# Kernel optimization log

Hardware: AMD Instinct MI355X
Metric: run time of the kernel (lower is better)

Reference implementation:

```python
import jax, jax.numpy as jnp
import numpy as np

COUNTS = (16, 8, 8)  # num_scale_layers from __init__


def _conv1d(x, w, b):
    # x: [B, C, L], w: [Cout, Cin, K] (torch Conv1d layout), valid padding, stride 1
    y = jax.lax.conv_general_dilated(
        x, w, window_strides=(1,), padding='VALID',
        dimension_numbers=('NCH', 'OIH', 'NCH'))
    return y + b[None, :, None]


def _maxpool3s2(x):
    # MaxPool1d(kernel=3, stride=2), valid padding
    return jax.lax.reduce_window(x, -jnp.inf, jax.lax.max,
                                 (1, 1, 3), (1, 1, 2), 'VALID')


def setup_inputs() -> dict:
    key = jax.random.key(0)
    ks = jax.random.split(key, 5)
    B, C, N = 64, 512, 64
    scale = 0.03  # ~1/sqrt(C*K), keeps deep relu-conv chain numerically sane
    x = jax.random.normal(ks[0], (B, C, N), jnp.float32)
    w1 = jax.random.normal(ks[1], (C, C, 1), jnp.float32) * scale
    b1 = jax.random.normal(ks[2], (C,), jnp.float32) * scale
    n_k2 = sum(COUNTS) - len(COUNTS)  # 29 kernel-size-2 convs
    w2 = jax.random.normal(ks[3], (n_k2, C, C, 2), jnp.float32) * scale
    b2 = jax.random.normal(ks[4], (n_k2, C), jnp.float32) * scale
    return {"x": x, "w1": w1, "b1": b1, "w2": w2, "b2": b2}


def reference(x, w1, b1, w2, b2):
    B, C, N = x.shape
    x2d = jnp.zeros((B, C, N, N), x.dtype)
    mask = np.eye(N, dtype=bool)  # static: indices are compile-time constants
    k2 = 0
    stride, offset = 1, 0
    for level, count in enumerate(COUNTS):
        for order in range(count):
            if level == 0 and order == 0:
                x = jax.nn.relu(_conv1d(x, w1, b1))
            elif level > 0 and order == 0:
                x = jax.nn.relu(_maxpool3s2(x))
            else:
                x = jax.nn.relu(_conv1d(x, w2[k2], b2[k2]))
                k2 += 1
            i = np.arange(0, N - offset, stride)
            j = np.arange(offset, N, stride)
            # scatter conv output onto strided diagonal of the 2D map
            x2d = x2d.at[:, :, i, j].set(x)
            mask[i, j] = True
            offset += stride
        offset += stride
        stride *= 2
    return x2d, jnp.asarray(mask)
```

## Files before the change

### kernel.cpp

```cpp
#include <hip/hip_runtime.h>

typedef _Float16 f16;
typedef f16 f16x8 __attribute__((ext_vector_type(8)));
typedef f16 f16x4 __attribute__((ext_vector_type(4)));
typedef f16 f16x2 __attribute__((ext_vector_type(2)));
typedef float f32x4 __attribute__((ext_vector_type(4)));

#define B_ 64
#define C_ 512
#define X2D_ELEMS ((size_t)134217728)
#define CHAIN_PITCH 1104

__device__ __forceinline__ int col_of(int i, int j) {
    const int d = j - i;
    if (d < 0) return -1;
    if (d <= 15) return 64 * d - (d * (d - 1)) / 2 + i;
    if (d >= 17 && d <= 31 && (d & 1) && !(i & 1)) {
        const int v = (d - 17) >> 1;
        return 904 + 24 * v - (v * (v - 1)) / 2 + (i >> 1);
    }
    if (d >= 35 && !((d - 35) & 3) && !(i & 3)) {
        const int v = (d - 35) >> 2;
        return 1068 + 8 * v - (v * (v - 1)) / 2 + (i >> 2);
    }
    return -1;
}

template<int K, int TAPS>
__global__ __launch_bounds__(256, 2)
void conv_fused(const f16* __restrict__ xin, int in_pitch, int cb_in,
                const f16* __restrict__ Wl, const float* __restrict__ bias,
                f16* __restrict__ chain, int cb_out,
                int Lin, int Lout, int G)
{
    __shared__ f16 Bs[64 * 512];
    const int tid = threadIdx.x, lane = tid & 63, wv = tid >> 6;
    const int b0 = blockIdx.x * G, m0 = blockIdx.y * 64;
    const int rows = G * Lin;

    for (int r = wv; r < rows; r += 4) {
        const int g = r / Lin, l = r - g * Lin;
        const f16* src = xin + (((size_t)(b0 + g) * in_pitch + cb_in + l) << 9);
        const f16x8 v = *(const f16x8*)(src + (lane << 3));
        *(f16x8*)&Bs[(r << 9) + ((lane ^ (r & 7)) << 3)] = v;
    }

    int vg[4], vl[4], row0[4]; bool val[4];
    #pragma unroll
    for (int nf = 0; nf < 4; nf++) {
        const int v = nf * 16 + (lane & 15);
        vg[nf] = v / Lout; vl[nf] = v - vg[nf] * Lout;
        val[nf] = vg[nf] < G;
        row0[nf] = val[nf] ? vg[nf] * Lin + vl[nf] : 0;
    }
    const int kg = lane >> 4;
    const f16* wp = Wl + (size_t)(m0 + wv * 16 + (lane & 15)) * K + (kg << 3);

    __syncthreads();

    f32x4 acc[4] = {};
    #pragma unroll 4
    for (int k0 = 0; k0 < K; k0 += 32) {
        const f16x8 af = *(const f16x8*)(wp + k0);
        const int t = (TAPS == 2 && k0 >= 512) ? 1 : 0;
        const int cchunk = (((TAPS == 2) ? (k0 & 511) : k0) >> 3) + kg;
        #pragma unroll
        for (int nf = 0; nf < 4; nf++) {
            const int r = row0[nf] + t;
            const f16x8 bf = *(const f16x8*)&Bs[(r << 9) + ((cchunk ^ (r & 7)) << 3)];
            acc[nf] = __builtin_amdgcn_mfma_f32_16x16x32_f16(af, bf, acc[nf], 0, 0, 0);
        }
    }

    const int co0 = m0 + wv * 16 + ((lane >> 4) << 2);
    const float4 bb = *(const float4*)&bias[co0];
    #pragma unroll
    for (int nf = 0; nf < 4; nf++) {
        if (!val[nf]) continue;
        f16x4 h;
        #pragma unroll
        for (int j = 0; j < 4; j++)
            h[j] = (f16)fmaxf(acc[nf][j] + ((const float*)&bb)[j], 0.0f);
        *(f16x4*)&chain[(((size_t)(b0 + vg[nf]) * CHAIN_PITCH + cb_out + vl[nf]) << 9) + co0] = h;
    }
}

__global__ void maxpool2(f16* __restrict__ chain, int cb_in, int cb_out)
{
    const int l = blockIdx.x, b = blockIdx.y, tid = threadIdx.x;
    const f16* s = chain + (((size_t)b * CHAIN_PITCH + cb_in + 2 * l) << 9) + 2 * tid;
    f16x2 o;
    o[0] = (f16)fmaxf(fmaxf(fmaxf((float)s[0], (float)s[512]), (float)s[1024]), 0.0f);
    o[1] = (f16)fmaxf(fmaxf(fmaxf((float)s[1], (float)s[513]), (float)s[1025]), 0.0f);
    *(f16x2*)&chain[(((size_t)b * CHAIN_PITCH + cb_out + l) << 9) + 2 * tid] = o;
}

__global__ void mask_kernel(float* __restrict__ mout)
{
    const int t = blockIdx.x * 256 + threadIdx.x;
    const int i = t >> 6, j = t & 63;
    mout[t] = (col_of(i, j) >= 0) ? 1.0f : 0.0f;
}

__global__ void wprep(const float* __restrict__ w1, const float* __restrict__ w2,
                      f16* __restrict__ Wf)
{
    size_t idx = (size_t)blockIdx.x * 256 + threadIdx.x;
    if (idx < 262144) {
        Wf[idx] = (f16)w1[idx];
    } else {
        idx -= 262144;
        const int k2 = idx >> 18;
        const int rem = idx & 262143;
        const int co = rem >> 9, ci = rem & 511;
        const float2 v = *(const float2*)&w2[((((size_t)k2 << 9) + co) << 10) + (ci << 1)];
        f16* base = Wf + 262144 + ((size_t)k2 << 19) + ((size_t)co << 10);
        base[ci] = (f16)v.x;
        base[512 + ci] = (f16)v.y;
    }
}

__global__ __launch_bounds__(256)
void xtrans(const float* __restrict__ x, f16* __restrict__ xT)
{
    __shared__ f16 t[64][20];
    const int s = blockIdx.x, b = blockIdx.y, tid = threadIdx.x;
    const int ci = tid >> 4, l0 = (tid & 15) << 2;
    const float4 v = *(const float4*)&x[(((size_t)b * C_ + s * 16 + ci) << 6) + l0];
    t[l0 + 0][ci] = (f16)v.x; t[l0 + 1][ci] = (f16)v.y;
    t[l0 + 2][ci] = (f16)v.z; t[l0 + 3][ci] = (f16)v.w;
    __syncthreads();
    const int l = tid >> 2, q = tid & 3;
    const f16x4 o = *(const f16x4*)&t[l][q << 2];
    *(f16x4*)&xT[((((size_t)b << 6) + l) << 9) + (s << 4) + (q << 2)] = o;
}

__global__ __launch_bounds__(256)
void assemble3(const f16* __restrict__ chain, float* __restrict__ x2d)
{
    __shared__ f16 J[64 * 512];
    const int tid = threadIdx.x, lane = tid & 63, wv = tid >> 6;
    const int i = blockIdx.x, b = blockIdx.y;

    for (int j = wv; j < 64; j += 4) {
        const int col = col_of(i, j);
        f16x8 v = {0, 0, 0, 0, 0, 0, 0, 0};
        if (col >= 0)
            v = *(const f16x8*)(chain + (((size_t)b * CHAIN_PITCH + col) << 9) + (lane << 3));
        *(f16x8*)&J[(j << 9) + ((lane ^ (j & 7)) << 3)] = v;
    }
    __syncthreads();

    const int jq = tid & 15, c0 = tid >> 4;
    float* dst0 = x2d + (((size_t)b * C_) << 12) + (i << 6) + (jq << 2);
    for (int ct = 0; ct < 32; ct++) {
        const int c = c0 + (ct << 4);
        const int cj = c >> 3;
        float4 o;
        #pragma unroll
        for (int jj = 0; jj < 4; jj++) {
            const int j = (jq << 2) + jj;
            ((float*)&o)[jj] = (float)J[(j << 9) + ((cj ^ (j & 7)) << 3) + (c & 7)];
        }
        *(float4*)(dst0 + ((size_t)c << 12)) = o;
    }
}

extern "C" void kernel_launch(void* const* d_in, const int* in_sizes, int n_in,
                              void* d_out, int out_size, void* d_ws, size_t ws_size,
                              hipStream_t stream)
{
    const float* x  = (const float*)d_in[0];
    const float* w1 = (const float*)d_in[1];
    const float* b1 = (const float*)d_in[2];
    const float* w2 = (const float*)d_in[3];
    const float* b2 = (const float*)d_in[4];
    float* x2d   = (float*)d_out;
    float* maskp = x2d + X2D_ELEMS;

    f16* chain = (f16*)d_ws;
    f16* Wf = (f16*)x2d;
    f16* xT = Wf + 262144 + (size_t)29 * 524288;

    mask_kernel<<<16, 256, 0, stream>>>(maskp);
    wprep<<<(30 * 262144) / 256, 256, 0, stream>>>(w1, w2, Wf);
    xtrans<<<dim3(32, B_), 256, 0, stream>>>(x, xT);

    const int counts[3] = {16, 8, 8};
    int L = 64, k2 = 0, cb = 0, prev = 0;
    for (int level = 0; level < 3; level++) {
        for (int order = 0; order < counts[level]; order++) {
            if (level == 0 && order == 0) {
                conv_fused<512, 1><<<dim3(64, 8), 256, 0, stream>>>(
                    xT, 64, 0, Wf, b1, chain, cb, 64, 64, 1);
            } else if (level > 0 && order == 0) {
                const int Lp = (L - 3) / 2 + 1;
                maxpool2<<<dim3(Lp, B_), 256, 0, stream>>>(chain, prev, cb);
                L = Lp;
            } else {
                const int Lout = L - 1;
                int G = 1;
                while ((G * 2) * Lout <= 64 && (G * 2) * L <= 64) G *= 2;
                conv_fused<1024, 2><<<dim3(64 / G, 8), 256, 0, stream>>>(
                    chain, CHAIN_PITCH, prev,
                    Wf + 262144 + (size_t)k2 * 524288, b2 + (size_t)k2 * C_,
                    chain, cb, L, Lout, G);
                k2++; L = Lout;
            }
            prev = cb; cb += L;
        }
    }
    assemble3<<<dim3(64, B_), 256, 0, stream>>>(chain, x2d);
}
```

Measured before the change: 652.0 us.

## Fuse all stages into one persistent cooperative kernel with grid syncs

```diff
diff --git a/kernel.cpp b/kernel.cpp
--- a/kernel.cpp
+++ b/kernel.cpp
@@ -1,4 +1,7 @@
 #include <hip/hip_runtime.h>
+#include <hip/hip_cooperative_groups.h>
+
+namespace cg = cooperative_groups;
 
 typedef _Float16 f16;
 typedef f16 f16x8 __attribute__((ext_vector_type(8)));
@@ -26,25 +29,20 @@
     return -1;
 }
 
-template<int K, int TAPS>
-__global__ __launch_bounds__(256, 2)
-void conv_fused(const f16* __restrict__ xin, int in_pitch, int cb_in,
-                const f16* __restrict__ Wl, const float* __restrict__ bias,
-                f16* __restrict__ chain, int cb_out,
-                int Lin, int Lout, int G)
-{
-    __shared__ f16 Bs[64 * 512];
+__device__ __forceinline__
+void conv_unit(f16* S, const f16* __restrict__ xin, int in_pitch, int cb_in,
+               const f16* __restrict__ Wl, const float* __restrict__ bias,
+               f16* __restrict__ chain, int cb_out,
+               int Lin, int Lout, int G, int K, int b0, int m0)
+{
     const int tid = threadIdx.x, lane = tid & 63, wv = tid >> 6;
-    const int b0 = blockIdx.x * G, m0 = blockIdx.y * 64;
     const int rows = G * Lin;
-
     for (int r = wv; r < rows; r += 4) {
         const int g = r / Lin, l = r - g * Lin;
         const f16* src = xin + (((size_t)(b0 + g) * in_pitch + cb_in + l) << 9);
         const f16x8 v = *(const f16x8*)(src + (lane << 3));
-        *(f16x8*)&Bs[(r << 9) + ((lane ^ (r & 7)) << 3)] = v;
-    }
-
+        *(f16x8*)&S[(r << 9) + ((lane ^ (r & 7)) << 3)] = v;
+    }
     int vg[4], vl[4], row0[4]; bool val[4];
     #pragma unroll
     for (int nf = 0; nf < 4; nf++) {
@@ -55,23 +53,20 @@
     }
     const int kg = lane >> 4;
     const f16* wp = Wl + (size_t)(m0 + wv * 16 + (lane & 15)) * K + (kg << 3);
-
     __syncthreads();
-
     f32x4 acc[4] = {};
     #pragma unroll 4
     for (int k0 = 0; k0 < K; k0 += 32) {
         const f16x8 af = *(const f16x8*)(wp + k0);
-        const int t = (TAPS == 2 && k0 >= 512) ? 1 : 0;
-        const int cchunk = (((TAPS == 2) ? (k0 & 511) : k0) >> 3) + kg;
+        const int t = (k0 >= 512) ? 1 : 0;
+        const int cchunk = ((k0 & 511) >> 3) + kg;
         #pragma unroll
         for (int nf = 0; nf < 4; nf++) {
             const int r = row0[nf] + t;
-            const f16x8 bf = *(const f16x8*)&Bs[(r << 9) + ((cchunk ^ (r & 7)) << 3)];
+            const f16x8 bf = *(const f16x8*)&S[(r << 9) + ((cchunk ^ (r & 7)) << 3)];
             acc[nf] = __builtin_amdgcn_mfma_f32_16x16x32_f16(af, bf, acc[nf], 0, 0, 0);
         }
     }
-
     const int co0 = m0 + wv * 16 + ((lane >> 4) << 2);
     const float4 bb = *(const float4*)&bias[co0];
     #pragma unroll
@@ -85,72 +80,19 @@
     }
 }
 
-__global__ void maxpool2(f16* __restrict__ chain, int cb_in, int cb_out)
-{
-    const int l = blockIdx.x, b = blockIdx.y, tid = threadIdx.x;
-    const f16* s = chain + (((size_t)b * CHAIN_PITCH + cb_in + 2 * l) << 9) + 2 * tid;
-    f16x2 o;
-    o[0] = (f16)fmaxf(fmaxf(fmaxf((float)s[0], (float)s[512]), (float)s[1024]), 0.0f);
-    o[1] = (f16)fmaxf(fmaxf(fmaxf((float)s[1], (float)s[513]), (float)s[1025]), 0.0f);
-    *(f16x2*)&chain[(((size_t)b * CHAIN_PITCH + cb_out + l) << 9) + 2 * tid] = o;
-}
-
-__global__ void mask_kernel(float* __restrict__ mout)
-{
-    const int t = blockIdx.x * 256 + threadIdx.x;
-    const int i = t >> 6, j = t & 63;
-    mout[t] = (col_of(i, j) >= 0) ? 1.0f : 0.0f;
-}
-
-__global__ void wprep(const float* __restrict__ w1, const float* __restrict__ w2,
-                      f16* __restrict__ Wf)
-{
-    size_t idx = (size_t)blockIdx.x * 256 + threadIdx.x;
-    if (idx < 262144) {
-        Wf[idx] = (f16)w1[idx];
-    } else {
-        idx -= 262144;
-        const int k2 = idx >> 18;
-        const int rem = idx & 262143;
-        const int co = rem >> 9, ci = rem & 511;
-        const float2 v = *(const float2*)&w2[((((size_t)k2 << 9) + co) << 10) + (ci << 1)];
-        f16* base = Wf + 262144 + ((size_t)k2 << 19) + ((size_t)co << 10);
-        base[ci] = (f16)v.x;
-        base[512 + ci] = (f16)v.y;
-    }
-}
-
-__global__ __launch_bounds__(256)
-void xtrans(const float* __restrict__ x, f16* __restrict__ xT)
-{
-    __shared__ f16 t[64][20];
-    const int s = blockIdx.x, b = blockIdx.y, tid = threadIdx.x;
-    const int ci = tid >> 4, l0 = (tid & 15) << 2;
-    const float4 v = *(const float4*)&x[(((size_t)b * C_ + s * 16 + ci) << 6) + l0];
-    t[l0 + 0][ci] = (f16)v.x; t[l0 + 1][ci] = (f16)v.y;
-    t[l0 + 2][ci] = (f16)v.z; t[l0 + 3][ci] = (f16)v.w;
-    __syncthreads();
-    const int l = tid >> 2, q = tid & 3;
-    const f16x4 o = *(const f16x4*)&t[l][q << 2];
-    *(f16x4*)&xT[((((size_t)b << 6) + l) << 9) + (s << 4) + (q << 2)] = o;
-}
-
-__global__ __launch_bounds__(256)
-void assemble3(const f16* __restrict__ chain, float* __restrict__ x2d)
-{
-    __shared__ f16 J[64 * 512];
+__device__ __forceinline__
+void assemble_unit(f16* S, const f16* __restrict__ chain, float* __restrict__ x2d,
+                   int i, int b)
+{
     const int tid = threadIdx.x, lane = tid & 63, wv = tid >> 6;
-    const int i = blockIdx.x, b = blockIdx.y;
-
     for (int j = wv; j < 64; j += 4) {
         const int col = col_of(i, j);
         f16x8 v = {0, 0, 0, 0, 0, 0, 0, 0};
         if (col >= 0)
             v = *(const f16x8*)(chain + (((size_t)b * CHAIN_PITCH + col) << 9) + (lane << 3));
-        *(f16x8*)&J[(j << 9) + ((lane ^ (j & 7)) << 3)] = v;
+        *(f16x8*)&S[(j << 9) + ((lane ^ (j & 7)) << 3)] = v;
     }
     __syncthreads();
-
     const int jq = tid & 15, c0 = tid >> 4;
     float* dst0 = x2d + (((size_t)b * C_) << 12) + (i << 6) + (jq << 2);
     for (int ct = 0; ct < 32; ct++) {
@@ -160,10 +102,162 @@
         #pragma unroll
         for (int jj = 0; jj < 4; jj++) {
             const int j = (jq << 2) + jj;
-            ((float*)&o)[jj] = (float)J[(j << 9) + ((cj ^ (j & 7)) << 3) + (c & 7)];
+            ((float*)&o)[jj] = (float)S[(j << 9) + ((cj ^ (j & 7)) << 3) + (c & 7)];
         }
         *(float4*)(dst0 + ((size_t)c << 12)) = o;
     }
+}
+
+__device__ __forceinline__
+void xtrans_unit(f16* S, const float* __restrict__ x, f16* __restrict__ xT,
+                 int s, int b)
+{
+    f16 (*t)[20] = (f16 (*)[20])S;
+    const int tid = threadIdx.x;
+    const int ci = tid >> 4, l0 = (tid & 15) << 2;
+    const float4 v = *(const float4*)&x[(((size_t)b * C_ + s * 16 + ci) << 6) + l0];
+    t[l0 + 0][ci] = (f16)v.x; t[l0 + 1][ci] = (f16)v.y;
+    t[l0 + 2][ci] = (f16)v.z; t[l0 + 3][ci] = (f16)v.w;
+    __syncthreads();
+    const int l = tid >> 2, q = tid & 3;
+    const f16x4 o = *(const f16x4*)&t[l][q << 2];
+    *(f16x4*)&xT[((((size_t)b << 6) + l) << 9) + (s << 4) + (q << 2)] = o;
+}
+
+__device__ __forceinline__
+void wprep_one(unsigned idx, const float* __restrict__ w1,
+               const float* __restrict__ w2, f16* __restrict__ Wf)
+{
+    if (idx < 262144u) {
+        Wf[idx] = (f16)w1[idx];
+    } else {
+        const unsigned r = idx - 262144u;
+        const int k2 = r >> 18;
+        const unsigned rem = r & 262143u;
+        const int co = rem >> 9, ci = rem & 511;
+        const float2 v = *(const float2*)&w2[((((size_t)k2 << 9) + co) << 10) + (ci << 1)];
+        f16* base = Wf + 262144 + ((size_t)k2 << 19) + ((size_t)co << 10);
+        base[ci] = (f16)v.x;
+        base[512 + ci] = (f16)v.y;
+    }
+}
+
+__global__ __launch_bounds__(256, 2)
+void persist(const float* __restrict__ x, const float* __restrict__ w1,
+             const float* __restrict__ b1, const float* __restrict__ w2,
+             const float* __restrict__ b2, f16* __restrict__ chain,
+             f16* __restrict__ Wf, f16* __restrict__ xT,
+             float* __restrict__ x2d, float* __restrict__ maskp)
+{
+    __shared__ __align__(16) f16 S[64 * 512];
+    cg::grid_group gg = cg::this_grid();
+    const int tid = threadIdx.x, bid = blockIdx.x, nB = gridDim.x;
+    const int gid = bid * 256 + tid, nT = nB * 256;
+
+    if (gid < 4096) maskp[gid] = (col_of(gid >> 6, gid & 63) >= 0) ? 1.0f : 0.0f;
+    for (unsigned idx = gid; idx < 30u * 262144u; idx += nT)
+        wprep_one(idx, w1, w2, Wf);
+    for (int u = bid; u < 2048; u += nB) {
+        __syncthreads();
+        xtrans_unit(S, x, xT, u & 31, u >> 5);
+    }
+    __threadfence();
+    gg.sync();
+
+    int L = 64, k2 = 0, cb = 0, prev = 0;
+    for (int level = 0; level < 3; level++) {
+        const int cnt = (level == 0) ? 16 : 8;
+        for (int order = 0; order < cnt; order++) {
+            if (level == 0 && order == 0) {
+                for (int u = bid; u < 512; u += nB) {
+                    __syncthreads();
+                    conv_unit(S, xT, 64, 0, Wf, b1, chain, cb,
+                              64, 64, 1, 512, u & 63, (u >> 6) << 6);
+                }
+            } else if (level > 0 && order == 0) {
+                const int Lp = (L - 3) / 2 + 1;
+                const int tot = B_ * Lp * 256;
+                for (int t = gid; t < tot; t += nT) {
+                    const int b = t / (Lp * 256);
+                    const int r = t - b * (Lp * 256);
+                    const int l = r >> 8, cp = r & 255;
+                    const f16* sp = chain + (((size_t)b * CHAIN_PITCH + prev + 2 * l) << 9) + 2 * cp;
+                    f16x2 o;
+                    o[0] = (f16)fmaxf(fmaxf(fmaxf((float)sp[0], (float)sp[512]), (float)sp[1024]), 0.0f);
+                    o[1] = (f16)fmaxf(fmaxf(fmaxf((float)sp[1], (float)sp[513]), (float)sp[1025]), 0.0f);
+                    *(f16x2*)&chain[(((size_t)b * CHAIN_PITCH + cb + l) << 9) + 2 * cp] = o;
+                }
+                L = Lp;
+            } else {
+                const int Lout = L - 1;
+                int G = 1;
+                while ((G * 2) * Lout <= 64 && (G * 2) * L <= 64) G *= 2;
+                const int ubg = 64 / G, units = ubg * 8;
+                const f16* Wl = Wf + 262144 + (size_t)k2 * 524288;
+                const float* bl = b2 + (size_t)k2 * C_;
+                for (int u = bid; u < units; u += nB) {
+                    __syncthreads();
+                    conv_unit(S, chain, CHAIN_PITCH, prev, Wl, bl, chain, cb,
+                              L, Lout, G, 1024, (u % ubg) * G, (u / ubg) << 6);
+                }
+                k2++; L = Lout;
+            }
+            prev = cb; cb += L;
+            __threadfence();
+            gg.sync();
+        }
+    }
+
+    for (int u = bid; u < 4096; u += nB) {
+        __syncthreads();
+        assemble_unit(S, chain, x2d, u & 63, u >> 6);
+    }
+}
+
+__global__ __launch_bounds__(256, 2)
+void conv_k(const f16* __restrict__ xin, int in_pitch, int cb_in,
+            const f16* __restrict__ Wl, const float* __restrict__ bias,
+            f16* __restrict__ chain, int cb_out, int Lin, int Lout, int G, int K)
+{
+    __shared__ __align__(16) f16 S[64 * 512];
+    conv_unit(S, xin, in_pitch, cb_in, Wl, bias, chain, cb_out,
+              Lin, Lout, G, K, blockIdx.x * G, blockIdx.y << 6);
+}
+
+__global__ void maxpool_kf(f16* __restrict__ chain, int cb_in, int cb_out)
+{
+    const int l = blockIdx.x, b = blockIdx.y, tid = threadIdx.x;
+    const f16* s = chain + (((size_t)b * CHAIN_PITCH + cb_in + 2 * l) << 9) + 2 * tid;
+    f16x2 o;
+    o[0] = (f16)fmaxf(fmaxf(fmaxf((float)s[0], (float)s[512]), (float)s[1024]), 0.0f);
+    o[1] = (f16)fmaxf(fmaxf(fmaxf((float)s[1], (float)s[513]), (float)s[1025]), 0.0f);
+    *(f16x2*)&chain[(((size_t)b * CHAIN_PITCH + cb_out + l) << 9) + 2 * tid] = o;
+}
+
+__global__ void mask_k(float* __restrict__ mout)
+{
+    const int t = blockIdx.x * 256 + threadIdx.x;
+    mout[t] = (col_of(t >> 6, t & 63) >= 0) ? 1.0f : 0.0f;
+}
+
+__global__ void wprep_k(const float* __restrict__ w1, const float* __restrict__ w2,
+                        f16* __restrict__ Wf)
+{
+    wprep_one((unsigned)(blockIdx.x * 256 + threadIdx.x), w1, w2, Wf);
+}
+
+__global__ __launch_bounds__(256)
+void xtrans_k(const float* __restrict__ x, f16* __restrict__ xT)
+{
+    __shared__ __align__(16) f16 S[64 * 20];
+    xtrans_unit(S, x, xT, blockIdx.x, blockIdx.y);
+}
+
+__global__ __launch_bounds__(256)
+void assemble_k(const f16* __restrict__ chain, float* __restrict__ x2d)
+{
+    __shared__ __align__(16) f16 S[64 * 512];
+    assemble_unit(S, chain, x2d, blockIdx.x, blockIdx.y);
 }
 
 extern "C" void kernel_launch(void* const* d_in, const int* in_sizes, int n_in,
@@ -182,33 +276,44 @@
     f16* Wf = (f16*)x2d;
     f16* xT = Wf + 262144 + (size_t)29 * 524288;
 
-    mask_kernel<<<16, 256, 0, stream>>>(maskp);
-    wprep<<<(30 * 262144) / 256, 256, 0, stream>>>(w1, w2, Wf);
-    xtrans<<<dim3(32, B_), 256, 0, stream>>>(x, xT);
+    int maxB = 0;
+    hipError_t oe = hipOccupancyMaxActiveBlocksPerMultiprocessor(
+        &maxB, (const void*)persist, 256, 0);
+    const int nB = (oe == hipSuccess && maxB >= 2) ? 512 : 256;
+
+    void* args[] = {(void*)&x, (void*)&w1, (void*)&b1, (void*)&w2, (void*)&b2,
+                    (void*)&chain, (void*)&Wf, (void*)&xT, (void*)&x2d, (void*)&maskp};
+    hipError_t le = hipLaunchCooperativeKernel((const void*)persist, dim3(nB),
+                                               dim3(256), args, 0, stream);
+    if (le == hipSuccess) return;
+
+    mask_k<<<16, 256, 0, stream>>>(maskp);
+    wprep_k<<<(30 * 262144) / 256, 256, 0, stream>>>(w1, w2, Wf);
+    xtrans_k<<<dim3(32, B_), 256, 0, stream>>>(x, xT);
 
     const int counts[3] = {16, 8, 8};
     int L = 64, k2 = 0, cb = 0, prev = 0;
     for (int level = 0; level < 3; level++) {
         for (int order = 0; order < counts[level]; order++) {
             if (level == 0 && order == 0) {
-                conv_fused<512, 1><<<dim3(64, 8), 256, 0, stream>>>(
-                    xT, 64, 0, Wf, b1, chain, cb, 64, 64, 1);
+                conv_k<<<dim3(64, 8), 256, 0, stream>>>(
+                    xT, 64, 0, Wf, b1, chain, cb, 64, 64, 1, 512);
             } else if (level > 0 && order == 0) {
                 const int Lp = (L - 3) / 2 + 1;
-                maxpool2<<<dim3(Lp, B_), 256, 0, stream>>>(chain, prev, cb);
+                maxpool_kf<<<dim3(Lp, B_), 256, 0, stream>>>(chain, prev, cb);
                 L = Lp;
             } else {
                 const int Lout = L - 1;
                 int G = 1;
                 while ((G * 2) * Lout <= 64 && (G * 2) * L <= 64) G *= 2;
-                conv_fused<1024, 2><<<dim3(64 / G, 8), 256, 0, stream>>>(
-                    chain, CHAIN_PITCH, prev,
-                    Wf + 262144 + (size_t)k2 * 524288, b2 + (size_t)k2 * C_,
-                    chain, cb, L, Lout, G);
+                conv_k<<<dim3(64 / G, 8), 256, 0, stream>>>(
+                    chain, CHAIN_PITCH, prev, Wf + 262144 + (size_t)k2 * 524288,
+                    b2 + (size_t)k2 * C_, chain, cb, L, Lout, G, 1024);
                 k2++; L = Lout;
             }
             prev = cb; cb += L;
         }
-    }
-    assemble3<<<dim3(64, B_), 256, 0, stream>>>(chain, x2d);
-}
+        L = L;
+    }
+    assemble_k<<<dim3(64, B_), 256, 0, stream>>>(chain, x2d);
+}
```

After: 2.565 ms. +293.4%, slower.

## Fuse entire conv/pool chain into one persistent per-batch kernel with LDS ping-pong

Applied to the files above, without the earlier changes.

```diff
diff --git a/kernel.cpp b/kernel.cpp
--- a/kernel.cpp
+++ b/kernel.cpp
@@ -3,7 +3,6 @@
 typedef _Float16 f16;
 typedef f16 f16x8 __attribute__((ext_vector_type(8)));
 typedef f16 f16x4 __attribute__((ext_vector_type(4)));
-typedef f16 f16x2 __attribute__((ext_vector_type(2)));
 typedef float f32x4 __attribute__((ext_vector_type(4)));
 
 #define B_ 64
@@ -26,92 +25,184 @@
     return -1;
 }
 
-template<int K, int TAPS>
-__global__ __launch_bounds__(256, 2)
-void conv_fused(const f16* __restrict__ xin, int in_pitch, int cb_in,
-                const f16* __restrict__ Wl, const float* __restrict__ bias,
-                f16* __restrict__ chain, int cb_out,
-                int Lin, int Lout, int G)
-{
-    __shared__ f16 Bs[64 * 512];
-    const int tid = threadIdx.x, lane = tid & 63, wv = tid >> 6;
-    const int b0 = blockIdx.x * G, m0 = blockIdx.y * 64;
-    const int rows = G * Lin;
-
-    for (int r = wv; r < rows; r += 4) {
-        const int g = r / Lin, l = r - g * Lin;
-        const f16* src = xin + (((size_t)(b0 + g) * in_pitch + cb_in + l) << 9);
-        const f16x8 v = *(const f16x8*)(src + (lane << 3));
-        *(f16x8*)&Bs[(r << 9) + ((lane ^ (r & 7)) << 3)] = v;
-    }
-
-    int vg[4], vl[4], row0[4]; bool val[4];
+template<int K, int NF, int TAPS>
+__device__ __forceinline__
+void conv_step(const f16* Scur, f16* Snxt,
+               const f16* __restrict__ wl, const float* __restrict__ bias,
+               f16* __restrict__ chout, int Lin, int Lout)
+{
+    const int tid = threadIdx.x, lane = tid & 63, w = tid >> 6;
+    const int colq = lane & 15, kg = lane >> 4;
+    const f16* wp = wl + (size_t)(w * 128 + colq) * K + (kg << 3);
+
+    int row[NF];
     #pragma unroll
-    for (int nf = 0; nf < 4; nf++) {
-        const int v = nf * 16 + (lane & 15);
-        vg[nf] = v / Lout; vl[nf] = v - vg[nf] * Lout;
-        val[nf] = vg[nf] < G;
-        row0[nf] = val[nf] ? vg[nf] * Lin + vl[nf] : 0;
-    }
-    const int kg = lane >> 4;
-    const f16* wp = Wl + (size_t)(m0 + wv * 16 + (lane & 15)) * K + (kg << 3);
-
+    for (int nf = 0; nf < NF; nf++) {
+        int c = nf * 16 + colq;
+        if (TAPS == 2 && c > Lin - 2) c = Lin - 2;
+        row[nf] = c;
+    }
+
+    f32x4 acc[8][NF] = {};
+    f16x8 afA[8], afB[8];
+    #pragma unroll
+    for (int m = 0; m < 8; m++) afA[m] = *(const f16x8*)(wp + (m << 4) * K);
+
+    for (int k0 = 0; k0 < K; k0 += 64) {
+        #pragma unroll
+        for (int m = 0; m < 8; m++)
+            afB[m] = *(const f16x8*)(wp + (m << 4) * K + k0 + 32);
+        {
+            const int t = (TAPS == 2 && k0 >= 512) ? 1 : 0;
+            const int cch = ((k0 & 511) >> 3) + kg;
+            f16x8 bf[NF];
+            #pragma unroll
+            for (int nf = 0; nf < NF; nf++) {
+                const int r = row[nf] + t;
+                bf[nf] = *(const f16x8*)&Scur[(r << 9) + ((cch ^ (r & 7)) << 3)];
+            }
+            #pragma unroll
+            for (int m = 0; m < 8; m++)
+                #pragma unroll
+                for (int nf = 0; nf < NF; nf++)
+                    acc[m][nf] = __builtin_amdgcn_mfma_f32_16x16x32_f16(
+                        afA[m], bf[nf], acc[m][nf], 0, 0, 0);
+        }
+        if (k0 + 64 < K) {
+            #pragma unroll
+            for (int m = 0; m < 8; m++)
+                afA[m] = *(const f16x8*)(wp + (m << 4) * K + k0 + 64);
+        }
+        {
+            const int k1 = k0 + 32;
+            const int t = (TAPS == 2 && k1 >= 512) ? 1 : 0;
+            const int cch = ((k1 & 511) >> 3) + kg;
+            f16x8 bf[NF];
+            #pragma unroll
+            for (int nf = 0; nf < NF; nf++) {
+                const int r = row[nf] + t;
+                bf[nf] = *(const f16x8*)&Scur[(r << 9) + ((cch ^ (r & 7)) << 3)];
+            }
+            #pragma unroll
+            for (int m = 0; m < 8; m++)
+                #pragma unroll
+                for (int nf = 0; nf < NF; nf++)
+                    acc[m][nf] = __builtin_amdgcn_mfma_f32_16x16x32_f16(
+                        afB[m], bf[nf], acc[m][nf], 0, 0, 0);
+        }
+    }
+
+    #pragma unroll
+    for (int m = 0; m < 8; m++) {
+        const int co = w * 128 + (m << 4) + (kg << 2);
+        const float4 bb = *(const float4*)&bias[co];
+        #pragma unroll
+        for (int nf = 0; nf < NF; nf++) {
+            const int col = nf * 16 + colq;
+            if (col < Lout) {
+                f16x4 h;
+                #pragma unroll
+                for (int j = 0; j < 4; j++)
+                    h[j] = (f16)fmaxf(acc[m][nf][j] + ((const float*)&bb)[j], 0.0f);
+                *(f16x4*)&Snxt[(col << 9) + ((((co >> 3) ^ (col & 7)) << 3) + (co & 7))] = h;
+                *(f16x4*)&chout[((size_t)col << 9) + co] = h;
+            }
+        }
+    }
+}
+
+__device__ __forceinline__
+void pool_step(const f16* Scur, f16* Snxt, f16* __restrict__ chout, int Lp)
+{
+    for (int u = threadIdx.x; u < Lp * 64; u += 256) {
+        const int l = u >> 6, c8 = u & 63;
+        const int r0 = 2 * l, r1 = r0 + 1, r2 = r0 + 2;
+        const f16x8 a = *(const f16x8*)&Scur[(r0 << 9) + ((c8 ^ (r0 & 7)) << 3)];
+        const f16x8 d = *(const f16x8*)&Scur[(r1 << 9) + ((c8 ^ (r1 & 7)) << 3)];
+        const f16x8 e = *(const f16x8*)&Scur[(r2 << 9) + ((c8 ^ (r2 & 7)) << 3)];
+        f16x8 o;
+        #pragma unroll
+        for (int j = 0; j < 8; j++)
+            o[j] = (f16)fmaxf(fmaxf((float)a[j], (float)d[j]), fmaxf((float)e[j], 0.0f));
+        *(f16x8*)&Snxt[(l << 9) + ((c8 ^ (l & 7)) << 3)] = o;
+        *(f16x8*)&chout[((size_t)l << 9) + (c8 << 3)] = o;
+    }
+}
+
+__global__ __launch_bounds__(256, 1)
+void chain_all(const float* __restrict__ x, const f16* __restrict__ Wf,
+               const float* __restrict__ b1, const float* __restrict__ b2,
+               f16* __restrict__ chain)
+{
+    __shared__ __align__(16) f16 S[2][64 * 512];
+    const int b = blockIdx.x, tid = threadIdx.x;
+    f16* chb = chain + (((size_t)b * CHAIN_PITCH) << 9);
+
+    for (int p = 0; p < 32; p++) {
+        const int ci = p * 16 + (tid >> 4), l0 = (tid & 15) << 2;
+        const float4 v = *(const float4*)&x[(((size_t)b * C_ + ci) << 6) + l0];
+        #pragma unroll
+        for (int j = 0; j < 4; j++) {
+            const int r = l0 + j;
+            S[0][(r << 9) + (((ci >> 3) ^ (r & 7)) << 3) + (ci & 7)] =
+                (f16)((const float*)&v)[j];
+        }
+    }
     __syncthreads();
 
-    f32x4 acc[4] = {};
-    #pragma unroll 4
-    for (int k0 = 0; k0 < K; k0 += 32) {
-        const f16x8 af = *(const f16x8*)(wp + k0);
-        const int t = (TAPS == 2 && k0 >= 512) ? 1 : 0;
-        const int cchunk = (((TAPS == 2) ? (k0 & 511) : k0) >> 3) + kg;
-        #pragma unroll
-        for (int nf = 0; nf < 4; nf++) {
-            const int r = row0[nf] + t;
-            const f16x8 bf = *(const f16x8*)&Bs[(r << 9) + ((cchunk ^ (r & 7)) << 3)];
-            acc[nf] = __builtin_amdgcn_mfma_f32_16x16x32_f16(af, bf, acc[nf], 0, 0, 0);
-        }
-    }
-
-    const int co0 = m0 + wv * 16 + ((lane >> 4) << 2);
-    const float4 bb = *(const float4*)&bias[co0];
-    #pragma unroll
-    for (int nf = 0; nf < 4; nf++) {
-        if (!val[nf]) continue;
-        f16x4 h;
-        #pragma unroll
-        for (int j = 0; j < 4; j++)
-            h[j] = (f16)fmaxf(acc[nf][j] + ((const float*)&bb)[j], 0.0f);
-        *(f16x4*)&chain[(((size_t)(b0 + vg[nf]) * CHAIN_PITCH + cb_out + vl[nf]) << 9) + co0] = h;
-    }
-}
-
-__global__ void maxpool2(f16* __restrict__ chain, int cb_in, int cb_out)
-{
-    const int l = blockIdx.x, b = blockIdx.y, tid = threadIdx.x;
-    const f16* s = chain + (((size_t)b * CHAIN_PITCH + cb_in + 2 * l) << 9) + 2 * tid;
-    f16x2 o;
-    o[0] = (f16)fmaxf(fmaxf(fmaxf((float)s[0], (float)s[512]), (float)s[1024]), 0.0f);
-    o[1] = (f16)fmaxf(fmaxf(fmaxf((float)s[1], (float)s[513]), (float)s[1025]), 0.0f);
-    *(f16x2*)&chain[(((size_t)b * CHAIN_PITCH + cb_out + l) << 9) + 2 * tid] = o;
-}
-
-__global__ void mask_kernel(float* __restrict__ mout)
-{
-    const int t = blockIdx.x * 256 + threadIdx.x;
-    const int i = t >> 6, j = t & 63;
-    mout[t] = (col_of(i, j) >= 0) ? 1.0f : 0.0f;
-}
-
-__global__ void wprep(const float* __restrict__ w1, const float* __restrict__ w2,
-                      f16* __restrict__ Wf)
-{
-    size_t idx = (size_t)blockIdx.x * 256 + threadIdx.x;
-    if (idx < 262144) {
+    int cur = 0, cb = 0, L = 64, k2 = 0;
+
+    conv_step<512, 4, 1>(S[0], S[1], Wf, b1, chb, 64, 64);
+    __syncthreads();
+    cur = 1; cb = 64;
+
+    for (int i = 0; i < 15; i++) {
+        const int Lout = L - 1;
+        conv_step<1024, 4, 2>(S[cur], S[cur ^ 1], Wf + 262144 + (size_t)k2 * 524288,
+                              b2 + k2 * C_, chb + ((size_t)cb << 9), L, Lout);
+        __syncthreads();
+        cur ^= 1; cb += Lout; L = Lout; k2++;
+    }
+    {
+        const int Lp = (L - 3) / 2 + 1;
+        pool_step(S[cur], S[cur ^ 1], chb + ((size_t)cb << 9), Lp);
+        __syncthreads();
+        cur ^= 1; cb += Lp; L = Lp;
+    }
+    for (int i = 0; i < 7; i++) {
+        const int Lout = L - 1;
+        conv_step<1024, 2, 2>(S[cur], S[cur ^ 1], Wf + 262144 + (size_t)k2 * 524288,
+                              b2 + k2 * C_, chb + ((size_t)cb << 9), L, Lout);
+        __syncthreads();
+        cur ^= 1; cb += Lout; L = Lout; k2++;
+    }
+    {
+        const int Lp = (L - 3) / 2 + 1;
+        pool_step(S[cur], S[cur ^ 1], chb + ((size_t)cb << 9), Lp);
+        __syncthreads();
+        cur ^= 1; cb += Lp; L = Lp;
+    }
+    for (int i = 0; i < 7; i++) {
+        const int Lout = L - 1;
+        conv_step<1024, 1, 2>(S[cur], S[cur ^ 1], Wf + 262144 + (size_t)k2 * 524288,
+                              b2 + k2 * C_, chb + ((size_t)cb << 9), L, Lout);
+        __syncthreads();
+        cur ^= 1; cb += Lout; L = Lout; k2++;
+    }
+}
+
+__global__ void prep_k(const float* __restrict__ w1, const float* __restrict__ w2,
+                       f16* __restrict__ Wf, float* __restrict__ maskp)
+{
+    const unsigned idx = blockIdx.x * 256 + threadIdx.x;
+    if (idx < 4096u)
+        maskp[idx] = (col_of(idx >> 6, idx & 63) >= 0) ? 1.0f : 0.0f;
+    if (idx < 262144u) {
         Wf[idx] = (f16)w1[idx];
-    } else {
-        idx -= 262144;
-        const int k2 = idx >> 18;
-        const int rem = idx & 262143;
+    } else if (idx < 30u * 262144u) {
+        const unsigned r = idx - 262144u;
+        const int k2 = r >> 18;
+        const unsigned rem = r & 262143u;
         const int co = rem >> 9, ci = rem & 511;
         const float2 v = *(const float2*)&w2[((((size_t)k2 << 9) + co) << 10) + (ci << 1)];
         f16* base = Wf + 262144 + ((size_t)k2 << 19) + ((size_t)co << 10);
@@ -121,24 +212,9 @@
 }
 
 __global__ __launch_bounds__(256)
-void xtrans(const float* __restrict__ x, f16* __restrict__ xT)
-{
-    __shared__ f16 t[64][20];
-    const int s = blockIdx.x, b = blockIdx.y, tid = threadIdx.x;
-    const int ci = tid >> 4, l0 = (tid & 15) << 2;
-    const float4 v = *(const float4*)&x[(((size_t)b * C_ + s * 16 + ci) << 6) + l0];
-    t[l0 + 0][ci] = (f16)v.x; t[l0 + 1][ci] = (f16)v.y;
-    t[l0 + 2][ci] = (f16)v.z; t[l0 + 3][ci] = (f16)v.w;
-    __syncthreads();
-    const int l = tid >> 2, q = tid & 3;
-    const f16x4 o = *(const f16x4*)&t[l][q << 2];
-    *(f16x4*)&xT[((((size_t)b << 6) + l) << 9) + (s << 4) + (q << 2)] = o;
-}
-
-__global__ __launch_bounds__(256)
-void assemble3(const f16* __restrict__ chain, float* __restrict__ x2d)
-{
-    __shared__ f16 J[64 * 512];
+void assemble_k(const f16* __restrict__ chain, float* __restrict__ x2d)
+{
+    __shared__ __align__(16) f16 S[64 * 512];
     const int tid = threadIdx.x, lane = tid & 63, wv = tid >> 6;
     const int i = blockIdx.x, b = blockIdx.y;
 
@@ -147,10 +223,9 @@
         f16x8 v = {0, 0, 0, 0, 0, 0, 0, 0};
         if (col >= 0)
             v = *(const f16x8*)(chain + (((size_t)b * CHAIN_PITCH + col) << 9) + (lane << 3));
-        *(f16x8*)&J[(j << 9) + ((lane ^ (j & 7)) << 3)] = v;
+        *(f16x8*)&S[(j << 9) + ((lane ^ (j & 7)) << 3)] = v;
     }
     __syncthreads();
-
     const int jq = tid & 15, c0 = tid >> 4;
     float* dst0 = x2d + (((size_t)b * C_) << 12) + (i << 6) + (jq << 2);
     for (int ct = 0; ct < 32; ct++) {
@@ -160,7 +235,7 @@
         #pragma unroll
         for (int jj = 0; jj < 4; jj++) {
             const int j = (jq << 2) + jj;
-            ((float*)&o)[jj] = (float)J[(j << 9) + ((cj ^ (j & 7)) << 3) + (c & 7)];
+            ((float*)&o)[jj] = (float)S[(j << 9) + ((cj ^ (j & 7)) << 3) + (c & 7)];
         }
         *(float4*)(dst0 + ((size_t)c << 12)) = o;
     }
@@ -180,35 +255,8 @@
 
     f16* chain = (f16*)d_ws;
     f16* Wf = (f16*)x2d;
-    f16* xT = Wf + 262144 + (size_t)29 * 524288;
-
-    mask_kernel<<<16, 256, 0, stream>>>(maskp);
-    wprep<<<(30 * 262144) / 256, 256, 0, stream>>>(w1, w2, Wf);
-    xtrans<<<dim3(32, B_), 256, 0, stream>>>(x, xT);
-
-    const int counts[3] = {16, 8, 8};
-    int L = 64, k2 = 0, cb = 0, prev = 0;
-    for (int level = 0; level < 3; level++) {
-        for (int order = 0; order < counts[level]; order++) {
-            if (level == 0 && order == 0) {
-                conv_fused<512, 1><<<dim3(64, 8), 256, 0, stream>>>(
-                    xT, 64, 0, Wf, b1, chain, cb, 64, 64, 1);
-            } else if (level > 0 && order == 0) {
-                const int Lp = (L - 3) / 2 + 1;
-                maxpool2<<<dim3(Lp, B_), 256, 0, stream>>>(chain, prev, cb);
-                L = Lp;
-            } else {
-                const int Lout = L - 1;
-                int G = 1;
-                while ((G * 2) * Lout <= 64 && (G * 2) * L <= 64) G *= 2;
-                conv_fused<1024, 2><<<dim3(64 / G, 8), 256, 0, stream>>>(
-                    chain, CHAIN_PITCH, prev,
-                    Wf + 262144 + (size_t)k2 * 524288, b2 + (size_t)k2 * C_,
-                    chain, cb, L, Lout, G);
-                k2++; L = Lout;
-            }
-            prev = cb; cb += L;
-        }
-    }
-    assemble3<<<dim3(64, B_), 256, 0, stream>>>(chain, x2d);
-}
+
+    prep_k<<<(30 * 262144) / 256, 256, 0, stream>>>(w1, w2, Wf, maskp);
+    chain_all<<<B_, 256, 0, stream>>>(x, Wf, b1, b2, chain);
+    assemble_k<<<dim3(64, B_), 256, 0, stream>>>(chain, x2d);
+}
```

After: 1.216 ms. 86.5% more time.
